# Optimization experiments

Hardware: AMD Instinct MI355X
Metric: run time of the kernel (lower is better)

## Reference

```python
import jax, jax.numpy as jnp
import numpy as np

NH = 8
DK = 64
DV = 64
FILTERS = 128


def conv1x1(x, w, b):
    # x: [B,C,H,W], w: [O,I,1,1]
    y = jax.lax.conv_general_dilated(x, w, (1, 1), 'VALID',
                                     dimension_numbers=('NCHW', 'OIHW', 'NCHW'))
    return y + b[None, :, None, None]


def rel_to_abs(x):
    # x: [B, N, L, 2L-1] relative logits -> [B, N, L, L] absolute logits
    B, N, L, _ = x.shape
    x = jnp.concatenate([x, jnp.zeros((B, N, L, 1), x.dtype)], axis=3)  # [B,N,L,2L]
    flat = x.reshape(B, N, L * 2 * L)
    flat = jnp.concatenate([flat, jnp.zeros((B, N, L - 1), x.dtype)], axis=2)
    final = flat.reshape(B, N, L + 1, 2 * L - 1)
    return final[:, :, :L, L - 1:]


def relative_logits_1d(q, rel_k):
    # q: [B,Nh,X,Y,d], rel_k: [2Y-1,d] -> [B,Nh,X,Y,Y]
    B, N, X, Y, _ = q.shape
    r = jnp.einsum('bnxyd,md->bnxym', q, rel_k)  # [B,Nh,X,Y,2Y-1]
    r = rel_to_abs(r.reshape(B, N * X, Y, 2 * Y - 1))  # [B,Nh*X,Y,Y]
    return r.reshape(B, N, X, Y, Y)


def setup_inputs() -> dict:
    key = jax.random.key(0)
    ks = jax.random.split(key, 10)
    B, C, H, W = 4, 64, 32, 32
    dkh = DK // NH
    s = lambda fan: 1.0 / np.sqrt(fan)
    x = jax.random.normal(ks[0], (B, C, H, W), jnp.float32)
    w_conv = jax.random.normal(ks[1], (FILTERS - DV, C, 1, 1), jnp.float32) * s(C)
    b_conv = jnp.zeros((FILTERS - DV,), jnp.float32)
    w_qkv = jax.random.normal(ks[2], (2 * DK + DV, C, 1, 1), jnp.float32) * s(C)
    b_qkv = jnp.zeros((2 * DK + DV,), jnp.float32)
    w_attn = jax.random.normal(ks[3], (DV, DV, 1, 1), jnp.float32) * s(DV)
    b_attn = jnp.zeros((DV,), jnp.float32)
    key_rel_h = jax.random.normal(ks[4], (2 * H - 1, dkh), jnp.float32) * s(dkh)
    key_rel_w = jax.random.normal(ks[5], (2 * W - 1, dkh), jnp.float32) * s(dkh)
    return {'x': x, 'w_conv': w_conv, 'b_conv': b_conv, 'w_qkv': w_qkv,
            'b_qkv': b_qkv, 'w_attn': w_attn, 'b_attn': b_attn,
            'key_rel_h': key_rel_h, 'key_rel_w': key_rel_w}


def reference(x, w_conv, b_conv, w_qkv, b_qkv, w_attn, b_attn, key_rel_h, key_rel_w):
    B, C, H, W = x.shape
    dkh, dvh = DK // NH, DV // NH
    HW = H * W

    conv_out = conv1x1(x, w_conv, b_conv)  # [B, filters-dv, H, W]

    qkv = conv1x1(x, w_qkv, b_qkv)  # [B, 2dk+dv, H, W]
    q, k, v = jnp.split(qkv, [DK, 2 * DK], axis=1)

    q = q.reshape(B, NH, dkh, H, W) * (dkh ** -0.5)
    k = k.reshape(B, NH, dkh, H, W)
    v = v.reshape(B, NH, dvh, H, W)

    flat_q = q.reshape(B, NH, dkh, HW).transpose(0, 1, 3, 2)  # [B,Nh,HW,dkh]
    flat_k = k.reshape(B, NH, dkh, HW).transpose(0, 1, 3, 2)
    flat_v = v.reshape(B, NH, dvh, HW).transpose(0, 1, 3, 2)

    logits = jnp.einsum('bnqd,bnkd->bnqk', flat_q, flat_k)  # [B,Nh,HW,HW]

    # relative position logits
    q5 = q.transpose(0, 1, 3, 4, 2)  # [B,Nh,H,W,dkh]
    # width: [B,Nh,H,W,W] -> broadcast over key-height
    Lw = relative_logits_1d(q5, key_rel_w)
    logits = logits + jnp.broadcast_to(
        Lw[:, :, :, :, None, :], (B, NH, H, W, H, W)).reshape(B, NH, HW, HW)
    # height: transpose q to [B,Nh,W,H,dkh], get [B,Nh,W,H,H], broadcast over key-width
    Lh = relative_logits_1d(q5.transpose(0, 1, 3, 2, 4), key_rel_h)
    Lh = Lh.transpose(0, 1, 3, 2, 4)  # [B,Nh,H,W,H]
    logits = logits + jnp.broadcast_to(
        Lh[:, :, :, :, :, None], (B, NH, H, W, H, W)).reshape(B, NH, HW, HW)

    weights = jax.nn.softmax(logits, axis=-1)
    attn = jnp.einsum('bnqk,bnkd->bnqd', weights, flat_v)  # [B,Nh,HW,dvh]
    attn = attn.transpose(0, 1, 3, 2).reshape(B, DV, H, W)
    attn_out = conv1x1(attn, w_attn, b_attn)  # [B,dv,H,W]

    return jnp.concatenate([conv_out, attn_out], axis=1)
```

## Files before the change

kernel.cpp:

```cpp
#include <hip/hip_runtime.h>
#include <math.h>

#define HW_ 1024

typedef __attribute__((ext_vector_type(4))) float   f32x4;
typedef __attribute__((ext_vector_type(8))) short   s16x8;

__device__ __forceinline__ unsigned bf16rne(float x) {
  unsigned u = __builtin_bit_cast(unsigned, x);
  u += 0x7FFF + ((u >> 16) & 1);
  return u >> 16;
}

__device__ __forceinline__ void store_oc(int oc, const float av[4],
    float* __restrict__ out, ushort* __restrict__ qbf, ushort* __restrict__ kbf,
    ushort* __restrict__ vtg, int b, int p)
{
  if (oc < 64) {
    float4 acc = make_float4(av[0], av[1], av[2], av[3]);
    *(float4*)(out + ((size_t)b * 128 + oc) * HW_ + p) = acc;
  } else if (oc < 128) {
    const float SC = 0.35355339059327373f * 1.4426950408889634f;
    int qc = oc - 64, n = qc >> 3, d = qc & 7, bn = b * 8 + n;
    #pragma unroll
    for (int i = 0; i < 4; ++i)
      qbf[((size_t)bn * HW_ + p + i) * 8 + d] = (ushort)bf16rne(av[i] * SC);
  } else if (oc < 192) {
    int kc = oc - 128, n = kc >> 3, d = kc & 7, bn = b * 8 + n;
    #pragma unroll
    for (int i = 0; i < 4; ++i)
      kbf[((size_t)bn * HW_ + p + i) * 8 + d] = (ushort)bf16rne(av[i]);
  } else {
    int vc = oc - 192, n = vc >> 3, d = vc & 7, bn = b * 8 + n;
    #pragma unroll
    for (int i = 0; i < 4; ++i)
      vtg[((size_t)bn * 8 + d) * HW_ + p + i] = (ushort)bf16rne(av[i]);
  }
}

__global__ __launch_bounds__(256) void k_convs(
    const float* __restrict__ x, const float* __restrict__ w_conv, const float* __restrict__ b_conv,
    const float* __restrict__ w_qkv, const float* __restrict__ b_qkv,
    float* __restrict__ out,
    ushort* __restrict__ qbf, ushort* __restrict__ kbf, ushort* __restrict__ vtg)
{
  int bid = blockIdx.x;
  int pt  = bid & 3;
  int ocp = (bid >> 2) & 31;
  int b   = bid >> 7;
  int tid = threadIdx.x;
  int oc0 = ocp * 8 + (tid >> 6) * 2;
  int oc1 = oc0 + 1;
  int p   = pt * 256 + (tid & 63) * 4;

  const float* wrow0; const float* wrow1;
  float bias0, bias1;
  if (oc0 < 64) { wrow0 = w_conv + oc0 * 64; bias0 = b_conv[oc0];
                  wrow1 = w_conv + oc1 * 64; bias1 = b_conv[oc1]; }
  else          { wrow0 = w_qkv + (oc0 - 64) * 64; bias0 = b_qkv[oc0 - 64];
                  wrow1 = w_qkv + (oc1 - 64) * 64; bias1 = b_qkv[oc1 - 64]; }

  float4 a00 = make_float4(bias0, bias0, bias0, bias0);
  float4 a01 = make_float4(0.f, 0.f, 0.f, 0.f);
  float4 a10 = make_float4(bias1, bias1, bias1, bias1);
  float4 a11 = make_float4(0.f, 0.f, 0.f, 0.f);
  const float* xb = x + (size_t)b * 64 * HW_ + p;
  #pragma unroll 16
  for (int ci = 0; ci < 32; ++ci) {
    float4 x0 = *(const float4*)(xb + (size_t)ci * HW_);
    float4 x1 = *(const float4*)(xb + (size_t)(ci + 32) * HW_);
    float w00 = wrow0[ci], w01 = wrow0[ci + 32];
    float w10 = wrow1[ci], w11 = wrow1[ci + 32];
    a00.x = fmaf(w00, x0.x, a00.x); a01.x = fmaf(w01, x1.x, a01.x);
    a00.y = fmaf(w00, x0.y, a00.y); a01.y = fmaf(w01, x1.y, a01.y);
    a00.z = fmaf(w00, x0.z, a00.z); a01.z = fmaf(w01, x1.z, a01.z);
    a00.w = fmaf(w00, x0.w, a00.w); a01.w = fmaf(w01, x1.w, a01.w);
    a10.x = fmaf(w10, x0.x, a10.x); a11.x = fmaf(w11, x1.x, a11.x);
    a10.y = fmaf(w10, x0.y, a10.y); a11.y = fmaf(w11, x1.y, a11.y);
    a10.z = fmaf(w10, x0.z, a10.z); a11.z = fmaf(w11, x1.z, a11.z);
    a10.w = fmaf(w10, x0.w, a10.w); a11.w = fmaf(w11, x1.w, a11.w);
  }
  float av0[4] = {a00.x + a01.x, a00.y + a01.y, a00.z + a01.z, a00.w + a01.w};
  float av1[4] = {a10.x + a11.x, a10.y + a11.y, a10.z + a11.z, a10.w + a11.w};
  store_oc(oc0, av0, out, qbf, kbf, vtg, b, p);
  store_oc(oc1, av1, out, qbf, kbf, vtg, b, p);
}

__global__ __launch_bounds__(512, 4) void k_attn(
    const ushort* __restrict__ qbf, const ushort* __restrict__ kbf, const ushort* __restrict__ vtg,
    const float* __restrict__ rel_h, const float* __restrict__ rel_w,
    float* __restrict__ aws)
{
  __shared__ float rhd[64 * 33];
  __shared__ float rwd[64 * 33];
  __shared__ ushort P_lds[8][16][128];
  __shared__ __align__(16) ushort K_lds[1024 * 8];
  __shared__ float mbuf[4][16], lbuf[4][16];
  __shared__ float obuf[4][16][8];

  int bid = blockIdx.x;
  int qt = bid & 15;
  int bn = bid >> 4;
  int b = bn >> 3, n = bn & 7;
  int tid = threadIdx.x;
  int lane = tid & 63;
  int w = tid >> 6;
  int qsub = w & 3, half = w >> 2;

  {
    const uint4* src = (const uint4*)(kbf + (size_t)bn * HW_ * 8);
    uint4* dst = (uint4*)K_lds;
    dst[tid]       = src[tid];
    dst[tid + 512] = src[tid + 512];
  }

  {
    int qr = tid >> 3, qu = tid & 7;
    const ushort* qp = qbf + ((size_t)bn * HW_ + qt * 64 + qr) * 8;
    float qf[8];
    #pragma unroll
    for (int d = 0; d < 8; ++d) qf[d] = __builtin_bit_cast(float, (unsigned)qp[d] << 16);
    int h = (qt * 64 + qr) >> 5, ww = qr & 31;
    #pragma unroll
    for (int s = 0; s < 4; ++s) {
      int idx = qu * 4 + s;
      const float* rp = rel_h + (idx - h + 31) * 8;
      float a = 0.f;
      #pragma unroll
      for (int d = 0; d < 8; ++d) a = fmaf(qf[d], rp[d], a);
      rhd[qr * 33 + idx] = a;
      const float* rq = rel_w + (idx - ww + 31) * 8;
      float c = 0.f;
      #pragma unroll
      for (int d = 0; d < 8; ++d) c = fmaf(qf[d], rq[d], c);
      rwd[qr * 33 + idx] = c;
    }
  }
  __syncthreads();

  int q = lane & 15, g = lane >> 4;
  int qr = qsub * 16 + q;

  s16x8 qfrag = {0,0,0,0,0,0,0,0};
  if (lane < 16)
    qfrag = *(const s16x8*)(qbf + ((size_t)bn * HW_ + qt * 64 + qsub * 16 + lane) * 8);

  float rw2[2][4];
  #pragma unroll
  for (int r = 0; r < 4; ++r) {
    rw2[0][r] = rwd[qr * 33 + g * 4 + r];
    rw2[1][r] = rwd[qr * 33 + 16 + g * 4 + r];
  }

  const ushort* vbase = vtg + (size_t)bn * 8 * HW_;

  s16x8 vone;
  #pragma unroll
  for (int e = 0; e < 8; ++e) vone[e] = (short)0x3F80;
  s16x8 vzero = {0,0,0,0,0,0,0,0};

  float m = -1e30f;
  f32x4 O = {0.f, 0.f, 0.f, 0.f};

  char* prow = (char*)&P_lds[w][0][0] + q * 256;
  int sw = (q & 7) << 4;

  #pragma unroll
  for (int bki = 0; bki < 4; ++bki) {
    int bk = half * 4 + bki;
    float rh4[4];
    #pragma unroll
    for (int j = 0; j < 4; ++j) rh4[j] = rhd[qr * 33 + bk * 4 + j];

    f32x4 s[8];
    __builtin_amdgcn_s_setprio(1);
    #pragma unroll
    for (int t = 0; t < 8; ++t) {
      f32x4 c;
      #pragma unroll
      for (int r = 0; r < 4; ++r) c[r] = rh4[t >> 1] + rw2[t & 1][r];
      s16x8 kf = {0,0,0,0,0,0,0,0};
      if (lane < 16)
        kf = *(const s16x8*)(K_lds + (size_t)(bk * 128 + t * 16 + lane) * 8);
      s[t] = __builtin_amdgcn_mfma_f32_16x16x32_bf16(kf, qfrag, c, 0, 0, 0);
    }
    __builtin_amdgcn_s_setprio(0);

    s16x8 vfr[4];
    #pragma unroll
    for (int km = 0; km < 4; ++km) {
      if (q < 8)      vfr[km] = *(const s16x8*)(vbase + (size_t)q * HW_ + bk * 128 + km * 32 + g * 8);
      else if (q == 8) vfr[km] = vone;
      else             vfr[km] = vzero;
    }

    float t8[8];
    #pragma unroll
    for (int t = 0; t < 8; ++t)
      t8[t] = fmaxf(fmaxf(s[t][0], s[t][1]), fmaxf(s[t][2], s[t][3]));
    float mx = fmaxf(fmaxf(fmaxf(t8[0], t8[1]), fmaxf(t8[2], t8[3])),
                     fmaxf(fmaxf(t8[4], t8[5]), fmaxf(t8[6], t8[7])));
    mx = fmaxf(mx, __shfl_xor(mx, 16));
    mx = fmaxf(mx, __shfl_xor(mx, 32));
    float mn = fmaxf(m, mx);
    float corr = __builtin_amdgcn_exp2f(m - mn);
    m = mn;

    #pragma unroll
    for (int t = 0; t < 8; ++t)
      #pragma unroll
      for (int r = 0; r < 4; ++r)
        s[t][r] = __builtin_amdgcn_exp2f(s[t][r] - mn);

    #pragma unroll
    for (int r = 0; r < 4; ++r) O[r] *= corr;

    #pragma unroll
    for (int t = 0; t < 8; ++t) {
      unsigned w0, w1;
      asm("v_cvt_pk_bf16_f32 %0, %1, %2" : "=v"(w0) : "v"(s[t][0]), "v"(s[t][1]));
      asm("v_cvt_pk_bf16_f32 %0, %1, %2" : "=v"(w1) : "v"(s[t][2]), "v"(s[t][3]));
      *(uint2*)(prow + (((t * 32 + g * 8) ^ sw))) = make_uint2(w0, w1);
    }
    asm volatile("s_waitcnt lgkmcnt(0)" ::: "memory");

    __builtin_amdgcn_s_setprio(1);
    #pragma unroll
    for (int km = 0; km < 4; ++km) {
      s16x8 pfrag = *(const s16x8*)(prow + ((km * 64 + g * 16) ^ sw));
      O = __builtin_amdgcn_mfma_f32_16x16x32_bf16(vfr[km], pfrag, O, 0, 0, 0);
    }
    __builtin_amdgcn_s_setprio(0);
  }

  float l = __shfl(O[0], 32 + q);

  if (half == 1) {
    if (g < 2) {
      #pragma unroll
      for (int r = 0; r < 4; ++r) obuf[qsub][q][g * 4 + r] = O[r];
    }
    if (lane < 16) { mbuf[qsub][lane] = m; lbuf[qsub][lane] = l; }
  }
  __syncthreads();
  if (half == 0 && g < 2) {
    float m2 = mbuf[qsub][q], l2 = lbuf[qsub][q];
    float mn = fmaxf(m, m2);
    float c1 = __builtin_amdgcn_exp2f(m - mn);
    float c2 = __builtin_amdgcn_exp2f(m2 - mn);
    float inv = 1.f / (l * c1 + l2 * c2);
    int qrow = qt * 64 + qsub * 16 + q;
    float* ap = aws + ((size_t)b * 64 + n * 8) * HW_;
    #pragma unroll
    for (int r = 0; r < 4; ++r)
      ap[(size_t)(g * 4 + r) * HW_ + qrow] = (O[r] * c1 + obuf[qsub][q][g * 4 + r] * c2) * inv;
  }
}

__global__ __launch_bounds__(256) void k_attnconv(
    const float* __restrict__ aws, const float* __restrict__ w_attn, const float* __restrict__ b_attn,
    float* __restrict__ out)
{
  int bid = blockIdx.x;
  int pt  = bid & 3;
  int ocq = (bid >> 2) & 15;
  int b   = bid >> 6;
  int tid = threadIdx.x;
  int oc  = ocq * 4 + (tid >> 6);
  int p   = pt * 256 + (tid & 63) * 4;

  const float* wrow = w_attn + oc * 64;
  float bias = b_attn[oc];
  float4 acc = make_float4(bias, bias, bias, bias);
  const float* ab = aws + (size_t)b * 64 * HW_ + p;
  #pragma unroll 16
  for (int ci = 0; ci < 64; ++ci) {
    float wv = wrow[ci];
    float4 a4 = *(const float4*)(ab + (size_t)ci * HW_);
    acc.x = fmaf(wv, a4.x, acc.x);
    acc.y = fmaf(wv, a4.y, acc.y);
    acc.z = fmaf(wv, a4.z, acc.z);
    acc.w = fmaf(wv, a4.w, acc.w);
  }
  *(float4*)(out + ((size_t)b * 128 + 64 + oc) * HW_ + p) = acc;
}

extern "C" void kernel_launch(void* const* d_in, const int* in_sizes, int n_in,
                              void* d_out, int out_size, void* d_ws, size_t ws_size,
                              hipStream_t stream) {
  const float* x        = (const float*)d_in[0];
  const float* w_conv   = (const float*)d_in[1];
  const float* b_conv   = (const float*)d_in[2];
  const float* w_qkv    = (const float*)d_in[3];
  const float* b_qkv    = (const float*)d_in[4];
  const float* w_attn   = (const float*)d_in[5];
  const float* b_attn   = (const float*)d_in[6];
  const float* rel_h    = (const float*)d_in[7];
  const float* rel_w    = (const float*)d_in[8];
  float* out = (float*)d_out;

  float*  ws  = (float*)d_ws;
  float*  aws = ws;
  ushort* qbf = (ushort*)(ws + 262144);
  ushort* kbf = qbf + 262144;
  ushort* vtg = kbf + 262144;

  k_convs<<<512, 256, 0, stream>>>(x, w_conv, b_conv, w_qkv, b_qkv, out, qbf, kbf, vtg);
  k_attn<<<512, 512, 0, stream>>>(qbf, kbf, vtg, rel_h, rel_w, aws);
  k_attnconv<<<256, 256, 0, stream>>>(aws, w_attn, b_attn, out);
}
```

Before: 40.04 us.

## Stage V in swizzled LDS, store rel logits as bf16, split-K attn conv

The attention kernel now copies each head's V slice into XOR-swizzled shared memory once per block, so V fragments are read from LDS instead of global memory inside the key loop. The relative-position logits are kept in LDS as bf16 with a padded stride, which shrinks the LDS footprint and adds rounding error to the bias terms. The final 1x1 conv splits its 64 input channels across two half-waves, combines them with a cross-lane shuffle, and doubles the grid to 512 blocks for more parallelism. The extra 16 KB of LDS for V may reduce how many attention blocks fit on a CU.

```diff
diff --git a/kernel.cpp b/kernel.cpp
--- a/kernel.cpp
+++ b/kernel.cpp
@@ -10,6 +10,9 @@
   unsigned u = __builtin_bit_cast(unsigned, x);
   u += 0x7FFF + ((u >> 16) & 1);
   return u >> 16;
+}
+__device__ __forceinline__ float bf2f(ushort u) {
+  return __builtin_bit_cast(float, (unsigned)u << 16);
 }
 
 __device__ __forceinline__ void store_oc(int oc, const float av[4],
@@ -91,10 +94,11 @@
     const float* __restrict__ rel_h, const float* __restrict__ rel_w,
     float* __restrict__ aws)
 {
-  __shared__ float rhd[64 * 33];
-  __shared__ float rwd[64 * 33];
+  __shared__ ushort rhd[64 * 36];
+  __shared__ ushort rwd[64 * 36];
   __shared__ ushort P_lds[8][16][128];
   __shared__ __align__(16) ushort K_lds[1024 * 8];
+  __shared__ __align__(16) ushort V_lds[1024 * 8];
   __shared__ float mbuf[4][16], lbuf[4][16];
   __shared__ float obuf[4][16][8];
 
@@ -108,10 +112,15 @@
   int qsub = w & 3, half = w >> 2;
 
   {
-    const uint4* src = (const uint4*)(kbf + (size_t)bn * HW_ * 8);
-    uint4* dst = (uint4*)K_lds;
-    dst[tid]       = src[tid];
-    dst[tid + 512] = src[tid + 512];
+    const uint4* ksrc = (const uint4*)(kbf + (size_t)bn * HW_ * 8);
+    const uint4* vsrc = (const uint4*)(vtg + (size_t)bn * 8 * HW_);
+    uint4* kdst = (uint4*)K_lds;
+    uint4* vdst = (uint4*)V_lds;
+    kdst[tid]       = ksrc[tid];
+    kdst[tid + 512] = ksrc[tid + 512];
+    int g0 = tid, g1 = tid + 512;
+    vdst[(g0 & ~127) | ((g0 & 127) ^ ((g0 >> 7) & 7))] = vsrc[g0];
+    vdst[(g1 & ~127) | ((g1 & 127) ^ ((g1 >> 7) & 7))] = vsrc[g1];
   }
 
   {
@@ -119,7 +128,7 @@
     const ushort* qp = qbf + ((size_t)bn * HW_ + qt * 64 + qr) * 8;
     float qf[8];
     #pragma unroll
-    for (int d = 0; d < 8; ++d) qf[d] = __builtin_bit_cast(float, (unsigned)qp[d] << 16);
+    for (int d = 0; d < 8; ++d) qf[d] = bf2f(qp[d]);
     int h = (qt * 64 + qr) >> 5, ww = qr & 31;
     #pragma unroll
     for (int s = 0; s < 4; ++s) {
@@ -128,12 +137,12 @@
       float a = 0.f;
       #pragma unroll
       for (int d = 0; d < 8; ++d) a = fmaf(qf[d], rp[d], a);
-      rhd[qr * 33 + idx] = a;
+      rhd[qr * 36 + idx] = (ushort)bf16rne(a);
       const float* rq = rel_w + (idx - ww + 31) * 8;
       float c = 0.f;
       #pragma unroll
       for (int d = 0; d < 8; ++d) c = fmaf(qf[d], rq[d], c);
-      rwd[qr * 33 + idx] = c;
+      rwd[qr * 36 + idx] = (ushort)bf16rne(c);
     }
   }
   __syncthreads();
@@ -148,11 +157,9 @@
   float rw2[2][4];
   #pragma unroll
   for (int r = 0; r < 4; ++r) {
-    rw2[0][r] = rwd[qr * 33 + g * 4 + r];
-    rw2[1][r] = rwd[qr * 33 + 16 + g * 4 + r];
-  }
-
-  const ushort* vbase = vtg + (size_t)bn * 8 * HW_;
+    rw2[0][r] = bf2f(rwd[qr * 36 + g * 4 + r]);
+    rw2[1][r] = bf2f(rwd[qr * 36 + 16 + g * 4 + r]);
+  }
 
   s16x8 vone;
   #pragma unroll
@@ -170,7 +177,7 @@
     int bk = half * 4 + bki;
     float rh4[4];
     #pragma unroll
-    for (int j = 0; j < 4; ++j) rh4[j] = rhd[qr * 33 + bk * 4 + j];
+    for (int j = 0; j < 4; ++j) rh4[j] = bf2f(rhd[qr * 36 + bk * 4 + j]);
 
     f32x4 s[8];
     __builtin_amdgcn_s_setprio(1);
@@ -189,7 +196,9 @@
     s16x8 vfr[4];
     #pragma unroll
     for (int km = 0; km < 4; ++km) {
-      if (q < 8)      vfr[km] = *(const s16x8*)(vbase + (size_t)q * HW_ + bk * 128 + km * 32 + g * 8);
+      if (q < 8)
+        vfr[km] = *(const s16x8*)((const char*)V_lds + q * 2048 +
+                                  (((bk * 16 + km * 4 + g) ^ q) << 4));
       else if (q == 8) vfr[km] = vone;
       else             vfr[km] = vzero;
     }
@@ -262,19 +271,21 @@
     float* __restrict__ out)
 {
   int bid = blockIdx.x;
-  int pt  = bid & 3;
-  int ocq = (bid >> 2) & 15;
-  int b   = bid >> 6;
+  int pt  = bid & 7;
+  int ocq = (bid >> 3) & 15;
+  int b   = bid >> 7;
   int tid = threadIdx.x;
+  int lane = tid & 63;
   int oc  = ocq * 4 + (tid >> 6);
-  int p   = pt * 256 + (tid & 63) * 4;
-
-  const float* wrow = w_attn + oc * 64;
-  float bias = b_attn[oc];
-  float4 acc = make_float4(bias, bias, bias, bias);
-  const float* ab = aws + (size_t)b * 64 * HW_ + p;
+  int hf  = lane >> 5;
+  int p   = pt * 128 + (lane & 31) * 4;
+  int ci0 = hf * 32;
+
+  const float* wrow = w_attn + oc * 64 + ci0;
+  const float* ab = aws + (size_t)b * 64 * HW_ + (size_t)ci0 * HW_ + p;
+  float4 acc = make_float4(0.f, 0.f, 0.f, 0.f);
   #pragma unroll 16
-  for (int ci = 0; ci < 64; ++ci) {
+  for (int ci = 0; ci < 32; ++ci) {
     float wv = wrow[ci];
     float4 a4 = *(const float4*)(ab + (size_t)ci * HW_);
     acc.x = fmaf(wv, a4.x, acc.x);
@@ -282,7 +293,15 @@
     acc.z = fmaf(wv, a4.z, acc.z);
     acc.w = fmaf(wv, a4.w, acc.w);
   }
-  *(float4*)(out + ((size_t)b * 128 + 64 + oc) * HW_ + p) = acc;
+  acc.x += __shfl_xor(acc.x, 32);
+  acc.y += __shfl_xor(acc.y, 32);
+  acc.z += __shfl_xor(acc.z, 32);
+  acc.w += __shfl_xor(acc.w, 32);
+  if (hf == 0) {
+    float bias = b_attn[oc];
+    float4 r = make_float4(acc.x + bias, acc.y + bias, acc.z + bias, acc.w + bias);
+    *(float4*)(out + ((size_t)b * 128 + 64 + oc) * HW_ + p) = r;
+  }
 }
 
 extern "C" void kernel_launch(void* const* d_in, const int* in_sizes, int n_in,
@@ -307,5 +326,5 @@
 
   k_convs<<<512, 256, 0, stream>>>(x, w_conv, b_conv, w_qkv, b_qkv, out, qbf, kbf, vtg);
   k_attn<<<512, 512, 0, stream>>>(qbf, kbf, vtg, rel_h, rel_w, aws);
-  k_attnconv<<<256, 256, 0, stream>>>(aws, w_attn, b_attn, out);
-}
+  k_attnconv<<<512, 256, 0, stream>>>(aws, w_attn, b_attn, out);
+}
```

After: 38.22 us. 4.5% less time.
